# Kernel tuning notes

Hardware: AMD Instinct MI355X
Metric: run time of the kernel (lower is better)

Reference implementation:

```python
import jax, jax.numpy as jnp
import numpy as np
from jax import lax

H = 64  # hidden_size == embedding_size


def gru_last_hidden(emb, W_ih, W_hh, b_ih, b_hh):
    """PyTorch single-layer GRU over seq [L, H]; returns final hidden [H].
    Gate order in stacked weights: r, z, n (PyTorch convention)."""
    def step(h, x):
        gi = W_ih @ x + b_ih            # [3H]
        gh = W_hh @ h + b_hh            # [3H]
        i_r, i_z, i_n = jnp.split(gi, 3)
        h_r, h_z, h_n = jnp.split(gh, 3)
        r = jax.nn.sigmoid(i_r + h_r)
        z = jax.nn.sigmoid(i_z + h_z)
        n = jnp.tanh(i_n + r * h_n)
        h_new = (1.0 - z) * n + z * h
        return h_new, None
    h0 = jnp.zeros((H,), dtype=emb.dtype)
    h_last, _ = lax.scan(step, h0, emb)
    return h_last


def setup_inputs() -> dict:
    key = jax.random.key(0)
    ks = jax.random.split(key, 12)
    N, D, A, V, L = 256, 128, 40, 128, 16
    F3_IN = N * (D + H + N)
    s = 0.02
    return {
        "obs": jax.random.normal(ks[0], (N, D), dtype=jnp.float32),
        "token_ids": jax.random.randint(ks[1], (L,), 0, V),
        "emb_table": jax.random.normal(ks[2], (V, H), dtype=jnp.float32) * s,
        "gru_Wih": jax.random.normal(ks[3], (3 * H, H), dtype=jnp.float32) * s,
        "gru_Whh": jax.random.normal(ks[4], (3 * H, H), dtype=jnp.float32) * s,
        "gru_bih": jnp.zeros((3 * H,), dtype=jnp.float32),
        "gru_bhh": jnp.zeros((3 * H,), dtype=jnp.float32),
        "f1_W": jax.random.normal(ks[5], (H, 2 * D), dtype=jnp.float32) * s,
        "f1_b": jnp.zeros((H,), dtype=jnp.float32),
        "f3_W1": jax.random.normal(ks[6], (512, F3_IN), dtype=jnp.float32) * s,
        "f3_b1": jnp.zeros((512,), dtype=jnp.float32),
        "f3_W2": jax.random.normal(ks[7], (A, 512), dtype=jnp.float32) * s,
        "f3_b2": jnp.zeros((A,), dtype=jnp.float32),
    }


def reference(obs, token_ids, emb_table, gru_Wih, gru_Whh, gru_bih, gru_bhh,
              f1_W, f1_b, f3_W1, f3_b1, f3_W2, f3_b2):
    N = obs.shape[0]
    # Encoder: embedding lookup + GRU, keep last timestep output
    emb = emb_table[token_ids]                       # [L, H]
    g_tilde = gru_last_hidden(emb, gru_Wih, gru_Whh, gru_bih, gru_bhh)  # [H]

    # Pairwise f1 + dot with g_tilde. f1(concat(o_i,o_j)) @ g = obs_i@Wa.T@g
    # + obs_j@Wb.T@g + b@g  (exact factorization of the linear over pairs).
    Wa, Wb = jnp.split(f1_W, 2, axis=1)              # each [H, D]
    u = obs @ (Wa.T @ g_tilde)                       # [N]  (outer index a)
    v = obs @ (Wb.T @ g_tilde)                       # [N]  (inner index b)
    Z = u[:, None] + v[None, :] + jnp.dot(f1_b, g_tilde)   # [N, N]

    # softmax over ALL N^2 entries (torch Softmax(dim=0) on the flat stack)
    p = jax.nn.softmax(Z.reshape(-1)).reshape(N, N)

    g_rep = jnp.broadcast_to(g_tilde, (N, H))
    x = jnp.concatenate([obs, g_rep, p], axis=1).reshape(-1)  # [N*(D+H+N)]

    h1 = jax.nn.relu(f3_W1 @ x + f3_b1)
    return f3_W2 @ h1 + f3_b2                         # [action_shape]
```

## Files before the change

kernel.cpp:

```cpp
#include <hip/hip_runtime.h>
#include <math.h>

#define H    64
#define N    256
#define D    128
#define L    16
#define ROW  (D + H + N)
#define F3IN (N * ROW)
#define F3IN4 (F3IN / 4)
#define CHUNK4 (F3IN4 / 4)

__device__ __forceinline__ float sigmoidf_(float x) {
    return 1.0f / (1.0f + expf(-x));
}

__global__ __launch_bounds__(256) void k_enc_softmax(
    const int* __restrict__ token_ids, const float* __restrict__ emb_table,
    const float* __restrict__ Wih, const float* __restrict__ Whh,
    const float* __restrict__ bih, const float* __restrict__ bhh,
    const float* __restrict__ f1W, const float* __restrict__ obs,
    float* __restrict__ g_out, float* __restrict__ eu_out,
    float* __restrict__ ev_out, float* __restrict__ scale_out)
{
    __shared__ float emb[L][H];
    __shared__ float h[H];
    __shared__ float hnew[H];
    __shared__ float gi_s[3 * H];
    __shared__ float gh_s[3 * H];
    __shared__ float wa_s[D];
    __shared__ float wb_s[D];
    __shared__ float red[256];

    const int k = threadIdx.x;

    for (int idx = k; idx < L * H; idx += 256) {
        int t = idx >> 6, d = idx & 63;
        emb[t][d] = emb_table[token_ids[t] * H + d];
    }
    if (k < H) h[k] = 0.0f;

    float4 wih4[16], whh4[16];
    float bi = 0.0f, bh = 0.0f;
    if (k < 3 * H) {
        const float4* wi = (const float4*)(Wih + k * H);
        const float4* wh = (const float4*)(Whh + k * H);
#pragma unroll
        for (int c = 0; c < 16; ++c) { wih4[c] = wi[c]; whh4[c] = wh[c]; }
        bi = bih[k]; bh = bhh[k];
    }
    __syncthreads();

    for (int t = 0; t < L; ++t) {
        if (k < 3 * H) {
            const float4* et = (const float4*)emb[t];
            const float4* hv = (const float4*)h;
            float gi = bi, gh = bh;
#pragma unroll
            for (int c = 0; c < 16; ++c) {
                float4 e = et[c], hh = hv[c];
                gi += wih4[c].x * e.x + wih4[c].y * e.y + wih4[c].z * e.z + wih4[c].w * e.w;
                gh += whh4[c].x * hh.x + whh4[c].y * hh.y + whh4[c].z * hh.z + whh4[c].w * hh.w;
            }
            gi_s[k] = gi;
            gh_s[k] = gh;
        }
        __syncthreads();
        if (k < H) {
            float r = sigmoidf_(gi_s[k] + gh_s[k]);
            float z = sigmoidf_(gi_s[H + k] + gh_s[H + k]);
            float n = tanhf(gi_s[2 * H + k] + r * gh_s[2 * H + k]);
            hnew[k] = (1.0f - z) * n + z * h[k];
        }
        __syncthreads();
        if (k < H) h[k] = hnew[k];
        __syncthreads();
    }

    {
        float s = 0.0f;
#pragma unroll 8
        for (int kk = 0; kk < H; ++kk) s += f1W[kk * (2 * D) + k] * h[kk];
        if (k < D) wa_s[k] = s;
        else       wb_s[k - D] = s;
        if (k < H) g_out[k] = h[k];
    }
    __syncthreads();

    const float4* rowp = (const float4*)(obs + k * D);
    const float4* wav = (const float4*)wa_s;
    const float4* wbv = (const float4*)wb_s;
    float u = 0.0f, v = 0.0f;
#pragma unroll
    for (int c = 0; c < D / 4; ++c) {
        float4 o = rowp[c], a = wav[c], b = wbv[c];
        u += o.x * a.x + o.y * a.y + o.z * a.z + o.w * a.w;
        v += o.x * b.x + o.y * b.y + o.z * b.z + o.w * b.w;
    }

    red[k] = u; __syncthreads();
    for (int s = 128; s > 0; s >>= 1) { if (k < s) red[k] = fmaxf(red[k], red[k + s]); __syncthreads(); }
    const float mu = red[0]; __syncthreads();
    const float eui = expf(u - mu);
    red[k] = eui; __syncthreads();
    for (int s = 128; s > 0; s >>= 1) { if (k < s) red[k] += red[k + s]; __syncthreads(); }
    const float Su = red[0]; __syncthreads();

    red[k] = v; __syncthreads();
    for (int s = 128; s > 0; s >>= 1) { if (k < s) red[k] = fmaxf(red[k], red[k + s]); __syncthreads(); }
    const float mv = red[0]; __syncthreads();
    const float evi = expf(v - mv);
    red[k] = evi; __syncthreads();
    for (int s = 128; s > 0; s >>= 1) { if (k < s) red[k] += red[k + s]; __syncthreads(); }
    const float Sv = red[0];

    eu_out[k] = eui;
    ev_out[k] = evi;
    if (k == 0) scale_out[0] = 1.0f / (Su * Sv);
}

__global__ __launch_bounds__(128) void k_buildx(
    const float* __restrict__ obs, const float* __restrict__ g,
    const float* __restrict__ eu, const float* __restrict__ ev,
    const float* __restrict__ scale, float* __restrict__ x)
{
    const int i = blockIdx.x;
    const int t = threadIdx.x;
    if (t >= ROW / 4) return;

    float4 val;
    if (t < D / 4) {
        val = ((const float4*)(obs + i * D))[t];
    } else if (t < (D + H) / 4) {
        val = ((const float4*)g)[t - D / 4];
    } else {
        float4 e = ((const float4*)ev)[t - (D + H) / 4];
        float s = eu[i] * scale[0];
        val = make_float4(e.x * s, e.y * s, e.z * s, e.w * s);
    }
    ((float4*)x)[i * (ROW / 4) + t] = val;
}

__global__ __launch_bounds__(256) void k_matvec1(
    const float* __restrict__ W1, const float* __restrict__ x,
    float* __restrict__ partial)
{
    const int bid   = blockIdx.x;
    const int row   = bid >> 2;
    const int chunk = bid & 3;

    const float4* w  = (const float4*)W1 + (size_t)row * F3IN4 + chunk * CHUNK4;
    const float4* xv = (const float4*)x + chunk * CHUNK4;

    float s0 = 0.0f, s1 = 0.0f;
    for (int c = threadIdx.x; c < CHUNK4; c += 512) {
        float4 a0 = w[c],       b0 = xv[c];
        float4 a1 = w[c + 256], b1 = xv[c + 256];
        s0 += a0.x * b0.x + a0.y * b0.y + a0.z * b0.z + a0.w * b0.w;
        s1 += a1.x * b1.x + a1.y * b1.y + a1.z * b1.z + a1.w * b1.w;
    }
    float sum = s0 + s1;

    __shared__ float red[256];
    red[threadIdx.x] = sum; __syncthreads();
    for (int s = 128; s > 0; s >>= 1) {
        if (threadIdx.x < s) red[threadIdx.x] += red[threadIdx.x + s];
        __syncthreads();
    }
    if (threadIdx.x == 0) partial[bid] = red[0];
}

__global__ __launch_bounds__(512) void k_finish(
    const float* __restrict__ partial, const float* __restrict__ b1,
    const float* __restrict__ W2, const float* __restrict__ b2,
    float* __restrict__ out)
{
    __shared__ float h1s[512];
    const int r = threadIdx.x;
    {
        const float4 p = ((const float4*)partial)[r];
        h1s[r] = fmaxf(p.x + p.y + p.z + p.w + b1[r], 0.0f);
    }
    __syncthreads();

    const int wave = r >> 6, lane = r & 63;
    for (int row = wave; row < 40; row += 8) {
        float s = 0.0f;
#pragma unroll
        for (int c = 0; c < 8; ++c) s += W2[row * 512 + lane + c * 64] * h1s[lane + c * 64];
#pragma unroll
        for (int off = 32; off > 0; off >>= 1) s += __shfl_down(s, off, 64);
        if (lane == 0) out[row] = s + b2[row];
    }
}

extern "C" void kernel_launch(void* const* d_in, const int* in_sizes, int n_in,
                              void* d_out, int out_size, void* d_ws, size_t ws_size,
                              hipStream_t stream)
{
    const float* obs       = (const float*)d_in[0];
    const int*   token_ids = (const int*)  d_in[1];
    const float* emb_table = (const float*)d_in[2];
    const float* Wih       = (const float*)d_in[3];
    const float* Whh       = (const float*)d_in[4];
    const float* bih       = (const float*)d_in[5];
    const float* bhh       = (const float*)d_in[6];
    const float* f1W       = (const float*)d_in[7];
    const float* W1        = (const float*)d_in[9];
    const float* b1        = (const float*)d_in[10];
    const float* W2        = (const float*)d_in[11];
    const float* b2        = (const float*)d_in[12];

    float* ws    = (float*)d_ws;
    float* g     = ws;
    float* eu    = ws + 64;
    float* ev    = ws + 320;
    float* scale = ws + 576;
    float* x     = ws + 640;
    float* part  = ws + 640 + F3IN;
    float* out   = (float*)d_out;

    k_enc_softmax<<<1, 256, 0, stream>>>(token_ids, emb_table, Wih, Whh, bih,
                                         bhh, f1W, obs, g, eu, ev, scale);
    k_buildx<<<N, 128, 0, stream>>>(obs, g, eu, ev, scale, x);
    k_matvec1<<<2048, 256, 0, stream>>>(W1, x, part);
    k_finish<<<1, 512, 0, stream>>>(part, b1, W2, b2, out);
}
```

Measured before the change: 76.66 us.

## Fuse x construction into matvec and overlap obs columns with GRU encoder

```diff
diff --git a/kernel.cpp b/kernel.cpp
--- a/kernel.cpp
+++ b/kernel.cpp
@@ -5,180 +5,200 @@
 #define N    256
 #define D    128
 #define L    16
-#define ROW  (D + H + N)
-#define F3IN (N * ROW)
-#define F3IN4 (F3IN / 4)
-#define CHUNK4 (F3IN4 / 4)
+#define ROWLEN 448
+#define F3IN (N * ROWLEN)
+#define ROW4 112
+#define NROWS 512
 
 __device__ __forceinline__ float sigmoidf_(float x) {
     return 1.0f / (1.0f + expf(-x));
 }
-
-__global__ __launch_bounds__(256) void k_enc_softmax(
+__device__ __forceinline__ float dot4(float4 a, float4 b) {
+    return a.x * b.x + a.y * b.y + a.z * b.z + a.w * b.w;
+}
+
+__global__ __launch_bounds__(256, 8) void k_obs_enc(
+    const float* __restrict__ W1, const float* __restrict__ obs,
     const int* __restrict__ token_ids, const float* __restrict__ emb_table,
     const float* __restrict__ Wih, const float* __restrict__ Whh,
     const float* __restrict__ bih, const float* __restrict__ bhh,
-    const float* __restrict__ f1W, const float* __restrict__ obs,
-    float* __restrict__ g_out, float* __restrict__ eu_out,
-    float* __restrict__ ev_out, float* __restrict__ scale_out)
-{
-    __shared__ float emb[L][H];
-    __shared__ float h[H];
-    __shared__ float hnew[H];
-    __shared__ float gi_s[3 * H];
-    __shared__ float gh_s[3 * H];
-    __shared__ float wa_s[D];
-    __shared__ float wb_s[D];
+    const float* __restrict__ f1W,
+    float* __restrict__ g_out, float* __restrict__ eus_out,
+    float* __restrict__ ev_out, float* __restrict__ partial_obs)
+{
+    __shared__ float smem[4416];
+    const int t = threadIdx.x;
+    const int bid = blockIdx.x;
+
+    if (bid == 0) {
+        float* emb_s  = smem;
+        float* gi_all = smem + 1024;
+        float* h_s    = smem + 4096;
+        float* hnew_s = smem + 4160;
+        float* gh_s   = smem + 4224;
+
+        for (int idx = t; idx < L * H; idx += 256) {
+            int tt = idx >> 6, d = idx & 63;
+            emb_s[idx] = emb_table[token_ids[tt] * H + d];
+        }
+        if (t < H) h_s[t] = 0.0f;
+        __syncthreads();
+
+        if (t < 3 * H) {
+            float gi[L];
+#pragma unroll
+            for (int tt = 0; tt < L; ++tt) gi[tt] = 0.0f;
+            const float4* wr = (const float4*)(Wih + t * H);
+#pragma unroll
+            for (int c = 0; c < 16; ++c) {
+                float4 w = wr[c];
+#pragma unroll
+                for (int tt = 0; tt < L; ++tt)
+                    gi[tt] += dot4(w, ((const float4*)(emb_s + tt * 64))[c]);
+            }
+            float b = bih[t];
+#pragma unroll
+            for (int tt = 0; tt < L; ++tt) gi_all[tt * 192 + t] = gi[tt] + b;
+        }
+        float bh = (t < 3 * H) ? bhh[t] : 0.0f;
+        __syncthreads();
+
+        for (int tt = 0; tt < L; ++tt) {
+            if (t < 3 * H) {
+                const float4* wr = (const float4*)(Whh + t * H);
+                float gh = bh;
+#pragma unroll
+                for (int c = 0; c < 16; ++c)
+                    gh += dot4(wr[c], ((const float4*)h_s)[c]);
+                gh_s[t] = gh;
+            }
+            __syncthreads();
+            if (t < H) {
+                float r = sigmoidf_(gi_all[tt * 192 + t] + gh_s[t]);
+                float z = sigmoidf_(gi_all[tt * 192 + 64 + t] + gh_s[64 + t]);
+                float n = tanhf(gi_all[tt * 192 + 128 + t] + r * gh_s[128 + t]);
+                hnew_s[t] = (1.0f - z) * n + z * h_s[t];
+            }
+            __syncthreads();
+            if (t < H) h_s[t] = hnew_s[t];
+            __syncthreads();
+        }
+
+        float* wa_s = smem + 1024;
+        float* wb_s = smem + 1152;
+        float* red  = smem + 1280;
+        {
+            float s = 0.0f;
+#pragma unroll 8
+            for (int kk = 0; kk < H; ++kk) s += f1W[kk * (2 * D) + t] * h_s[kk];
+            if (t < D) wa_s[t] = s;
+            else       wb_s[t - D] = s;
+        }
+        __syncthreads();
+
+        const float4* rowp = (const float4*)(obs + t * D);
+        float u = 0.0f, v = 0.0f;
+#pragma unroll
+        for (int c = 0; c < 32; ++c) {
+            float4 o = rowp[c];
+            u += dot4(o, ((const float4*)wa_s)[c]);
+            v += dot4(o, ((const float4*)wb_s)[c]);
+        }
+
+        red[t] = u; __syncthreads();
+        for (int s = 128; s > 0; s >>= 1) { if (t < s) red[t] = fmaxf(red[t], red[t + s]); __syncthreads(); }
+        const float mu = red[0]; __syncthreads();
+        const float eui = expf(u - mu);
+        red[t] = eui; __syncthreads();
+        for (int s = 128; s > 0; s >>= 1) { if (t < s) red[t] += red[t + s]; __syncthreads(); }
+        const float Su = red[0]; __syncthreads();
+
+        red[t] = v; __syncthreads();
+        for (int s = 128; s > 0; s >>= 1) { if (t < s) red[t] = fmaxf(red[t], red[t + s]); __syncthreads(); }
+        const float mv = red[0]; __syncthreads();
+        const float evi = expf(v - mv);
+        red[t] = evi; __syncthreads();
+        for (int s = 128; s > 0; s >>= 1) { if (t < s) red[t] += red[t + s]; __syncthreads(); }
+        const float Sv = red[0]; __syncthreads();
+
+        const float scale = 1.0f / (Su * Sv);
+        eus_out[t] = eui * scale;
+        ev_out[t]  = evi;
+        if (t < H) g_out[t] = h_s[t];
+    }
+
+    const int row = bid >> 2, q = bid & 3;
+    const float4* wbase = (const float4*)W1 + (size_t)row * (F3IN / 4)
+                        + (size_t)(q * 64) * ROW4;
+    const float4* obs4 = (const float4*)obs + (q * 64) * 32;
+
+    float sum = 0.0f;
+#pragma unroll
+    for (int k = 0; k < 8; ++k) {
+        int idx = t + k * 256;
+        int s = idx >> 5, c4 = idx & 31;
+        sum += dot4(wbase[s * ROW4 + c4], obs4[s * 32 + c4]);
+    }
+
+    float* red2 = smem + 1280;
+    __syncthreads();
+    red2[t] = sum; __syncthreads();
+    for (int s = 128; s > 0; s >>= 1) {
+        if (t < s) red2[t] += red2[t + s];
+        __syncthreads();
+    }
+    if (t == 0) partial_obs[bid] = red2[0];
+}
+
+__global__ __launch_bounds__(256, 8) void k_gp(
+    const float* __restrict__ W1, const float* __restrict__ g,
+    const float* __restrict__ eus, const float* __restrict__ ev,
+    float* __restrict__ partial_gp)
+{
+    __shared__ float g_s[64];
+    __shared__ float ev_s[256];
+    __shared__ float eu_s[64];
     __shared__ float red[256];
 
-    const int k = threadIdx.x;
-
-    for (int idx = k; idx < L * H; idx += 256) {
-        int t = idx >> 6, d = idx & 63;
-        emb[t][d] = emb_table[token_ids[t] * H + d];
-    }
-    if (k < H) h[k] = 0.0f;
-
-    float4 wih4[16], whh4[16];
-    float bi = 0.0f, bh = 0.0f;
-    if (k < 3 * H) {
-        const float4* wi = (const float4*)(Wih + k * H);
-        const float4* wh = (const float4*)(Whh + k * H);
-#pragma unroll
-        for (int c = 0; c < 16; ++c) { wih4[c] = wi[c]; whh4[c] = wh[c]; }
-        bi = bih[k]; bh = bhh[k];
-    }
+    const int t = threadIdx.x;
+    const int row = blockIdx.x >> 2, q = blockIdx.x & 3;
+
+    if (t < 64) { g_s[t] = g[t]; eu_s[t] = eus[q * 64 + t]; }
+    ev_s[t] = ev[t];
     __syncthreads();
 
-    for (int t = 0; t < L; ++t) {
-        if (k < 3 * H) {
-            const float4* et = (const float4*)emb[t];
-            const float4* hv = (const float4*)h;
-            float gi = bi, gh = bh;
-#pragma unroll
-            for (int c = 0; c < 16; ++c) {
-                float4 e = et[c], hh = hv[c];
-                gi += wih4[c].x * e.x + wih4[c].y * e.y + wih4[c].z * e.z + wih4[c].w * e.w;
-                gh += whh4[c].x * hh.x + whh4[c].y * hh.y + whh4[c].z * hh.z + whh4[c].w * hh.w;
-            }
-            gi_s[k] = gi;
-            gh_s[k] = gh;
-        }
-        __syncthreads();
-        if (k < H) {
-            float r = sigmoidf_(gi_s[k] + gh_s[k]);
-            float z = sigmoidf_(gi_s[H + k] + gh_s[H + k]);
-            float n = tanhf(gi_s[2 * H + k] + r * gh_s[2 * H + k]);
-            hnew[k] = (1.0f - z) * n + z * h[k];
-        }
-        __syncthreads();
-        if (k < H) h[k] = hnew[k];
-        __syncthreads();
-    }
-
-    {
-        float s = 0.0f;
-#pragma unroll 8
-        for (int kk = 0; kk < H; ++kk) s += f1W[kk * (2 * D) + k] * h[kk];
-        if (k < D) wa_s[k] = s;
-        else       wb_s[k - D] = s;
-        if (k < H) g_out[k] = h[k];
-    }
-    __syncthreads();
-
-    const float4* rowp = (const float4*)(obs + k * D);
-    const float4* wav = (const float4*)wa_s;
-    const float4* wbv = (const float4*)wb_s;
-    float u = 0.0f, v = 0.0f;
-#pragma unroll
-    for (int c = 0; c < D / 4; ++c) {
-        float4 o = rowp[c], a = wav[c], b = wbv[c];
-        u += o.x * a.x + o.y * a.y + o.z * a.z + o.w * a.w;
-        v += o.x * b.x + o.y * b.y + o.z * b.z + o.w * b.w;
-    }
-
-    red[k] = u; __syncthreads();
-    for (int s = 128; s > 0; s >>= 1) { if (k < s) red[k] = fmaxf(red[k], red[k + s]); __syncthreads(); }
-    const float mu = red[0]; __syncthreads();
-    const float eui = expf(u - mu);
-    red[k] = eui; __syncthreads();
-    for (int s = 128; s > 0; s >>= 1) { if (k < s) red[k] += red[k + s]; __syncthreads(); }
-    const float Su = red[0]; __syncthreads();
-
-    red[k] = v; __syncthreads();
-    for (int s = 128; s > 0; s >>= 1) { if (k < s) red[k] = fmaxf(red[k], red[k + s]); __syncthreads(); }
-    const float mv = red[0]; __syncthreads();
-    const float evi = expf(v - mv);
-    red[k] = evi; __syncthreads();
-    for (int s = 128; s > 0; s >>= 1) { if (k < s) red[k] += red[k + s]; __syncthreads(); }
-    const float Sv = red[0];
-
-    eu_out[k] = eui;
-    ev_out[k] = evi;
-    if (k == 0) scale_out[0] = 1.0f / (Su * Sv);
-}
-
-__global__ __launch_bounds__(128) void k_buildx(
-    const float* __restrict__ obs, const float* __restrict__ g,
-    const float* __restrict__ eu, const float* __restrict__ ev,
-    const float* __restrict__ scale, float* __restrict__ x)
-{
-    const int i = blockIdx.x;
-    const int t = threadIdx.x;
-    if (t >= ROW / 4) return;
-
-    float4 val;
-    if (t < D / 4) {
-        val = ((const float4*)(obs + i * D))[t];
-    } else if (t < (D + H) / 4) {
-        val = ((const float4*)g)[t - D / 4];
-    } else {
-        float4 e = ((const float4*)ev)[t - (D + H) / 4];
-        float s = eu[i] * scale[0];
-        val = make_float4(e.x * s, e.y * s, e.z * s, e.w * s);
-    }
-    ((float4*)x)[i * (ROW / 4) + t] = val;
-}
-
-__global__ __launch_bounds__(256) void k_matvec1(
-    const float* __restrict__ W1, const float* __restrict__ x,
-    float* __restrict__ partial)
-{
-    const int bid   = blockIdx.x;
-    const int row   = bid >> 2;
-    const int chunk = bid & 3;
-
-    const float4* w  = (const float4*)W1 + (size_t)row * F3IN4 + chunk * CHUNK4;
-    const float4* xv = (const float4*)x + chunk * CHUNK4;
-
-    float s0 = 0.0f, s1 = 0.0f;
-    for (int c = threadIdx.x; c < CHUNK4; c += 512) {
-        float4 a0 = w[c],       b0 = xv[c];
-        float4 a1 = w[c + 256], b1 = xv[c + 256];
-        s0 += a0.x * b0.x + a0.y * b0.y + a0.z * b0.z + a0.w * b0.w;
-        s1 += a1.x * b1.x + a1.y * b1.y + a1.z * b1.z + a1.w * b1.w;
-    }
-    float sum = s0 + s1;
-
-    __shared__ float red[256];
-    red[threadIdx.x] = sum; __syncthreads();
+    const float4* wbase = (const float4*)W1 + (size_t)row * (F3IN / 4)
+                        + (size_t)(q * 64) * ROW4 + 32;
+
+    float sum = 0.0f;
+#pragma unroll 4
+    for (int k = 0; k < 20; ++k) {
+        int idx = t + k * 256;
+        int s = idx / 80, c4 = idx - s * 80;
+        float4 w = wbase[s * ROW4 + c4];
+        if (c4 < 16) sum += dot4(w, ((const float4*)g_s)[c4]);
+        else         sum += dot4(w, ((const float4*)ev_s)[c4 - 16]) * eu_s[s];
+    }
+
+    red[t] = sum; __syncthreads();
     for (int s = 128; s > 0; s >>= 1) {
-        if (threadIdx.x < s) red[threadIdx.x] += red[threadIdx.x + s];
-        __syncthreads();
-    }
-    if (threadIdx.x == 0) partial[bid] = red[0];
+        if (t < s) red[t] += red[t + s];
+        __syncthreads();
+    }
+    if (t == 0) partial_gp[blockIdx.x] = red[0];
 }
 
 __global__ __launch_bounds__(512) void k_finish(
-    const float* __restrict__ partial, const float* __restrict__ b1,
-    const float* __restrict__ W2, const float* __restrict__ b2,
-    float* __restrict__ out)
+    const float* __restrict__ po, const float* __restrict__ pg,
+    const float* __restrict__ b1, const float* __restrict__ W2,
+    const float* __restrict__ b2, float* __restrict__ out)
 {
     __shared__ float h1s[512];
     const int r = threadIdx.x;
     {
-        const float4 p = ((const float4*)partial)[r];
-        h1s[r] = fmaxf(p.x + p.y + p.z + p.w + b1[r], 0.0f);
+        float4 a = ((const float4*)po)[r];
+        float4 b = ((const float4*)pg)[r];
+        h1s[r] = fmaxf(a.x + a.y + a.z + a.w + b.x + b.y + b.z + b.w + b1[r], 0.0f);
     }
     __syncthreads();
 
@@ -186,7 +206,8 @@
     for (int row = wave; row < 40; row += 8) {
         float s = 0.0f;
 #pragma unroll
-        for (int c = 0; c < 8; ++c) s += W2[row * 512 + lane + c * 64] * h1s[lane + c * 64];
+        for (int c = 0; c < 8; ++c)
+            s += W2[row * 512 + lane + c * 64] * h1s[lane + c * 64];
 #pragma unroll
         for (int off = 32; off > 0; off >>= 1) s += __shfl_down(s, off, 64);
         if (lane == 0) out[row] = s + b2[row];
@@ -210,18 +231,16 @@
     const float* W2        = (const float*)d_in[11];
     const float* b2        = (const float*)d_in[12];
 
-    float* ws    = (float*)d_ws;
-    float* g     = ws;
-    float* eu    = ws + 64;
-    float* ev    = ws + 320;
-    float* scale = ws + 576;
-    float* x     = ws + 640;
-    float* part  = ws + 640 + F3IN;
-    float* out   = (float*)d_out;
-
-    k_enc_softmax<<<1, 256, 0, stream>>>(token_ids, emb_table, Wih, Whh, bih,
-                                         bhh, f1W, obs, g, eu, ev, scale);
-    k_buildx<<<N, 128, 0, stream>>>(obs, g, eu, ev, scale, x);
-    k_matvec1<<<2048, 256, 0, stream>>>(W1, x, part);
-    k_finish<<<1, 512, 0, stream>>>(part, b1, W2, b2, out);
-}
+    float* ws  = (float*)d_ws;
+    float* g   = ws;
+    float* eus = ws + 64;
+    float* ev  = ws + 320;
+    float* po  = ws + 576;
+    float* pg  = ws + 2624;
+    float* out = (float*)d_out;
+
+    k_obs_enc<<<2048, 256, 0, stream>>>(W1, obs, token_ids, emb_table, Wih, Whh,
+                                        bih, bhh, f1W, g, eus, ev, po);
+    k_gp<<<2048, 256, 0, stream>>>(W1, g, eus, ev, pg);
+    k_finish<<<1, 512, 0, stream>>>(po, pg, b1, W2, b2, out);
+}
```

After: 104.2 us. 35.9% more time.

## Fuse x construction into W1 matvec and drop the materialized x buffer

Applied to the files above, without the earlier changes.

```diff
diff --git a/kernel.cpp b/kernel.cpp
--- a/kernel.cpp
+++ b/kernel.cpp
@@ -5,22 +5,28 @@
 #define N    256
 #define D    128
 #define L    16
-#define ROW  (D + H + N)
-#define F3IN (N * ROW)
-#define F3IN4 (F3IN / 4)
-#define CHUNK4 (F3IN4 / 4)
+#define SEG    448
+#define SEG4   112
+#define F3IN (N * SEG)
+#define CHUNK_SEGS 64
+#define CHUNK4 (CHUNK_SEGS * SEG4)
+
+typedef float v4f __attribute__((ext_vector_type(4)));
 
 __device__ __forceinline__ float sigmoidf_(float x) {
     return 1.0f / (1.0f + expf(-x));
 }
-
-__global__ __launch_bounds__(256) void k_enc_softmax(
+__device__ __forceinline__ float dot4(float4 a, float4 b) {
+    return a.x * b.x + a.y * b.y + a.z * b.z + a.w * b.w;
+}
+
+__global__ __launch_bounds__(256) void k_enc(
     const int* __restrict__ token_ids, const float* __restrict__ emb_table,
     const float* __restrict__ Wih, const float* __restrict__ Whh,
     const float* __restrict__ bih, const float* __restrict__ bhh,
     const float* __restrict__ f1W, const float* __restrict__ obs,
-    float* __restrict__ g_out, float* __restrict__ eu_out,
-    float* __restrict__ ev_out, float* __restrict__ scale_out)
+    float* __restrict__ g_out, float* __restrict__ eus_out,
+    float* __restrict__ ev_out)
 {
     __shared__ float emb[L][H];
     __shared__ float h[H];
@@ -57,9 +63,8 @@
             float gi = bi, gh = bh;
 #pragma unroll
             for (int c = 0; c < 16; ++c) {
-                float4 e = et[c], hh = hv[c];
-                gi += wih4[c].x * e.x + wih4[c].y * e.y + wih4[c].z * e.z + wih4[c].w * e.w;
-                gh += whh4[c].x * hh.x + whh4[c].y * hh.y + whh4[c].z * hh.z + whh4[c].w * hh.w;
+                gi += dot4(wih4[c], et[c]);
+                gh += dot4(whh4[c], hv[c]);
             }
             gi_s[k] = gi;
             gh_s[k] = gh;
@@ -92,9 +97,9 @@
     float u = 0.0f, v = 0.0f;
 #pragma unroll
     for (int c = 0; c < D / 4; ++c) {
-        float4 o = rowp[c], a = wav[c], b = wbv[c];
-        u += o.x * a.x + o.y * a.y + o.z * a.z + o.w * a.w;
-        v += o.x * b.x + o.y * b.y + o.z * b.z + o.w * b.w;
+        float4 o = rowp[c];
+        u += dot4(o, wav[c]);
+        v += dot4(o, wbv[c]);
     }
 
     red[k] = u; __syncthreads();
@@ -113,60 +118,63 @@
     for (int s = 128; s > 0; s >>= 1) { if (k < s) red[k] += red[k + s]; __syncthreads(); }
     const float Sv = red[0];
 
-    eu_out[k] = eui;
-    ev_out[k] = evi;
-    if (k == 0) scale_out[0] = 1.0f / (Su * Sv);
-}
-
-__global__ __launch_bounds__(128) void k_buildx(
-    const float* __restrict__ obs, const float* __restrict__ g,
-    const float* __restrict__ eu, const float* __restrict__ ev,
-    const float* __restrict__ scale, float* __restrict__ x)
-{
-    const int i = blockIdx.x;
+    eus_out[k] = eui * (1.0f / (Su * Sv));
+    ev_out[k]  = evi;
+}
+
+__global__ __launch_bounds__(256, 4) void k_mv(
+    const float* __restrict__ W1, const float* __restrict__ obs,
+    const float* __restrict__ g, const float* __restrict__ eus,
+    const float* __restrict__ ev, float* __restrict__ partial)
+{
+    __shared__ float g_s[64];
+    __shared__ float ev_s[256];
+    __shared__ float eu_s[64];
+    __shared__ float red[256];
+
     const int t = threadIdx.x;
-    if (t >= ROW / 4) return;
-
-    float4 val;
-    if (t < D / 4) {
-        val = ((const float4*)(obs + i * D))[t];
-    } else if (t < (D + H) / 4) {
-        val = ((const float4*)g)[t - D / 4];
-    } else {
-        float4 e = ((const float4*)ev)[t - (D + H) / 4];
-        float s = eu[i] * scale[0];
-        val = make_float4(e.x * s, e.y * s, e.z * s, e.w * s);
-    }
-    ((float4*)x)[i * (ROW / 4) + t] = val;
-}
-
-__global__ __launch_bounds__(256) void k_matvec1(
-    const float* __restrict__ W1, const float* __restrict__ x,
-    float* __restrict__ partial)
-{
-    const int bid   = blockIdx.x;
-    const int row   = bid >> 2;
-    const int chunk = bid & 3;
-
-    const float4* w  = (const float4*)W1 + (size_t)row * F3IN4 + chunk * CHUNK4;
-    const float4* xv = (const float4*)x + chunk * CHUNK4;
-
-    float s0 = 0.0f, s1 = 0.0f;
-    for (int c = threadIdx.x; c < CHUNK4; c += 512) {
-        float4 a0 = w[c],       b0 = xv[c];
-        float4 a1 = w[c + 256], b1 = xv[c + 256];
-        s0 += a0.x * b0.x + a0.y * b0.y + a0.z * b0.z + a0.w * b0.w;
-        s1 += a1.x * b1.x + a1.y * b1.y + a1.z * b1.z + a1.w * b1.w;
-    }
-    float sum = s0 + s1;
-
-    __shared__ float red[256];
-    red[threadIdx.x] = sum; __syncthreads();
+    const int row = blockIdx.x >> 2, q = blockIdx.x & 3;
+
+    if (t < 64) { g_s[t] = g[t]; eu_s[t] = eus[q * 64 + t]; }
+    ev_s[t] = ev[t];
+    __syncthreads();
+
+    const v4f* wb = (const v4f*)W1 + (size_t)row * (F3IN / 4) + (size_t)q * CHUNK4;
+    const float4* obs4 = (const float4*)obs + q * CHUNK_SEGS * (D / 4);
+
+    float a0 = 0.0f, a1 = 0.0f, a2 = 0.0f, a3 = 0.0f;
+#pragma unroll 7
+    for (int k = 0; k < 28; ++k) {
+        const int idx = t + k * 256;
+        const int seg = idx / SEG4;
+        const int c4  = idx - seg * SEG4;
+        v4f w = __builtin_nontemporal_load(wb + idx);
+        float4 o;
+        if (c4 < 32) {
+            o = obs4[seg * 32 + c4];
+        } else if (c4 < 48) {
+            o = ((const float4*)g_s)[c4 - 32];
+        } else {
+            float4 e = ((const float4*)ev_s)[c4 - 48];
+            float m = eu_s[seg];
+            o = make_float4(e.x * m, e.y * m, e.z * m, e.w * m);
+        }
+        float d = w[0] * o.x + w[1] * o.y + w[2] * o.z + w[3] * o.w;
+        switch (k & 3) {
+            case 0: a0 += d; break;
+            case 1: a1 += d; break;
+            case 2: a2 += d; break;
+            default: a3 += d; break;
+        }
+    }
+    float sum = (a0 + a1) + (a2 + a3);
+
+    red[t] = sum; __syncthreads();
     for (int s = 128; s > 0; s >>= 1) {
-        if (threadIdx.x < s) red[threadIdx.x] += red[threadIdx.x + s];
-        __syncthreads();
-    }
-    if (threadIdx.x == 0) partial[bid] = red[0];
+        if (t < s) red[t] += red[t + s];
+        __syncthreads();
+    }
+    if (t == 0) partial[blockIdx.x] = red[0];
 }
 
 __global__ __launch_bounds__(512) void k_finish(
@@ -177,7 +185,7 @@
     __shared__ float h1s[512];
     const int r = threadIdx.x;
     {
-        const float4 p = ((const float4*)partial)[r];
+        float4 p = ((const float4*)partial)[r];
         h1s[r] = fmaxf(p.x + p.y + p.z + p.w + b1[r], 0.0f);
     }
     __syncthreads();
@@ -186,7 +194,8 @@
     for (int row = wave; row < 40; row += 8) {
         float s = 0.0f;
 #pragma unroll
-        for (int c = 0; c < 8; ++c) s += W2[row * 512 + lane + c * 64] * h1s[lane + c * 64];
+        for (int c = 0; c < 8; ++c)
+            s += W2[row * 512 + lane + c * 64] * h1s[lane + c * 64];
 #pragma unroll
         for (int off = 32; off > 0; off >>= 1) s += __shfl_down(s, off, 64);
         if (lane == 0) out[row] = s + b2[row];
@@ -210,18 +219,15 @@
     const float* W2        = (const float*)d_in[11];
     const float* b2        = (const float*)d_in[12];
 
-    float* ws    = (float*)d_ws;
-    float* g     = ws;
-    float* eu    = ws + 64;
-    float* ev    = ws + 320;
-    float* scale = ws + 576;
-    float* x     = ws + 640;
-    float* part  = ws + 640 + F3IN;
-    float* out   = (float*)d_out;
-
-    k_enc_softmax<<<1, 256, 0, stream>>>(token_ids, emb_table, Wih, Whh, bih,
-                                         bhh, f1W, obs, g, eu, ev, scale);
-    k_buildx<<<N, 128, 0, stream>>>(obs, g, eu, ev, scale, x);
-    k_matvec1<<<2048, 256, 0, stream>>>(W1, x, part);
+    float* ws   = (float*)d_ws;
+    float* g    = ws;
+    float* eus  = ws + 64;
+    float* ev   = ws + 320;
+    float* part = ws + 576;
+    float* out  = (float*)d_out;
+
+    k_enc<<<1, 256, 0, stream>>>(token_ids, emb_table, Wih, Whh, bih, bhh,
+                                 f1W, obs, g, eus, ev);
+    k_mv<<<2048, 256, 0, stream>>>(W1, obs, g, eus, ev, part);
     k_finish<<<1, 512, 0, stream>>>(part, b1, W2, b2, out);
 }
```

Result: faster. 71.86 us (-6.3%).
